# Kernel tuning notes

Measured on AMD Instinct MI355X. Metric: run time of the kernel, lower is better.

The kernel has to match this reference:

```python
import jax, jax.numpy as jnp
import numpy as np

NEG_BIG = -9e15
ALPHA = 0.2  # LeakyReLU negative slope
B, N, F_IN, F_OUT = 8, 2048, 128, 128


def setup_inputs() -> dict:
    key = jax.random.key(0)
    k1, k2, k3, k4 = jax.random.split(key, 4)
    inp = jax.random.normal(k1, (B, N, F_IN), dtype=jnp.float32)
    adj = jax.random.randint(k2, (B, N, N), 0, 2, dtype=jnp.int32)
    W = 0.02 * jax.random.normal(k3, (F_OUT, F_IN), dtype=jnp.float32)  # nn.Linear weight [out,in]
    a = 0.02 * jax.random.normal(k4, (1, 2 * F_OUT), dtype=jnp.float32)  # attention vector [1, 2F]
    return {"input": inp, "adj": adj, "W": W, "a": a}


def reference(input, adj, W, a):
    # h = input @ W^T : [B, N, F_OUT]
    h = jnp.einsum("bnf,of->bno", input, W)
    f_out = h.shape[-1]
    # Decompose a . [h_i || h_j] = (h_i . a1) + (h_j . a2) -- same math as the
    # explicit repeat_interleave/repeat/cat, without the O(N^2 * 2F) tensor.
    a1 = a[0, :f_out]
    a2 = a[0, f_out:]
    s1 = h @ a1  # [B, N] score for source node i
    s2 = h @ a2  # [B, N] score for target node j
    e = jax.nn.leaky_relu(s1[:, :, None] + s2[:, None, :], negative_slope=ALPHA)  # [B,N,N]
    masked = jnp.where(adj > 0, e, NEG_BIG)
    attention = jax.nn.softmax(masked, axis=-1)
    # dropout p=0.0 (eval) -> identity
    h_prime = jnp.einsum("bnm,bmo->bno", attention, h)
    return h_prime
```

## Files before the change

kernel.cpp:

```cpp
#include <hip/hip_runtime.h>
#include <stdint.h>


#define B_ 8
#define N_ 2048
#define FD 128
#define ALPHA_ 0.2f
#define TJ 128
#define NCHUNK (N_ / TJ)

typedef __attribute__((ext_vector_type(8))) short short8;
typedef __attribute__((ext_vector_type(4))) float f32x4;

#define HCHUNK(o, jc) ((((o) * 16) + ((jc) ^ ((o) & 15))) * 8)

__device__ __forceinline__ float bf2f(unsigned short u) {
    union { uint32_t i; float f; } v; v.i = ((uint32_t)u) << 16; return v.f;
}
__device__ __forceinline__ unsigned short f2bf(float f) {
    union { float f; uint32_t i; } v; v.f = f;
    uint32_t x = v.i;
    uint32_t r = (x + 0x7fffu + ((x >> 16) & 1u)) >> 16;
    return (unsigned short)r;
}

__global__ __launch_bounds__(256) void gat_h(
    const float* __restrict__ x,
    const float* __restrict__ W,
    const float* __restrict__ a,
    unsigned short* __restrict__ hT,
    float* __restrict__ s1o, float* __restrict__ s2o)
{
    __shared__ __align__(16) unsigned short Wlds[FD * FD];

    const int bid = blockIdx.x;
    const int tid = threadIdx.x;
    const int w = tid >> 6;
    const int lane = tid & 63;
    const int m = lane & 15;
    const int quad = lane >> 4;
    const int arow = bid * 64 + w * 16 + m;

#pragma unroll
    for (int it = 0; it < 8; it++) {
        int cid = it * 256 + tid;
        int o = cid >> 4, kc = cid & 15;
        const float* wp = W + (size_t)o * FD + kc * 8;
        float4 w0 = *(const float4*)wp;
        float4 w1 = *(const float4*)(wp + 4);
        uint4 pk;
        pk.x = (uint32_t)f2bf(w0.x) | ((uint32_t)f2bf(w0.y) << 16);
        pk.y = (uint32_t)f2bf(w0.z) | ((uint32_t)f2bf(w0.w) << 16);
        pk.z = (uint32_t)f2bf(w1.x) | ((uint32_t)f2bf(w1.y) << 16);
        pk.w = (uint32_t)f2bf(w1.z) | ((uint32_t)f2bf(w1.w) << 16);
        *(uint4*)&Wlds[HCHUNK(o, kc)] = pk;
    }
    __syncthreads();

    f32x4 acc[8];
#pragma unroll
    for (int ot = 0; ot < 8; ot++) acc[ot] = (f32x4){0.f, 0.f, 0.f, 0.f};

#pragma unroll
    for (int ks = 0; ks < 4; ks++) {
        const float* xp = x + (size_t)arow * FD + ks * 32 + quad * 8;
        float4 x0 = *(const float4*)xp;
        float4 x1 = *(const float4*)(xp + 4);
        float xv[8] = {x0.x, x0.y, x0.z, x0.w, x1.x, x1.y, x1.z, x1.w};
        union { unsigned short us[8]; short8 v; } ahi, alo;
#pragma unroll
        for (int jj = 0; jj < 8; jj++) {
            unsigned short hi = f2bf(xv[jj]);
            ahi.us[jj] = hi;
            alo.us[jj] = f2bf(xv[jj] - bf2f(hi));
        }
#pragma unroll
        for (int ot = 0; ot < 8; ot++) {
            union { uint4 u; short8 v; } bw;
            bw.u = *(const uint4*)&Wlds[HCHUNK(ot * 16 + m, ks * 4 + quad)];
            acc[ot] = __builtin_amdgcn_mfma_f32_16x16x32_bf16(ahi.v, bw.v, acc[ot], 0, 0, 0);
            acc[ot] = __builtin_amdgcn_mfma_f32_16x16x32_bf16(alo.v, bw.v, acc[ot], 0, 0, 0);
        }
    }

    const int rc0 = bid * 64 + w * 16 + quad * 4;
    const int bb = rc0 >> 11;
    const int jb = rc0 & (N_ - 1);
    unsigned short* hTb = hT + (size_t)bb * FD * N_;
    float s1p[4] = {0.f, 0.f, 0.f, 0.f};
    float s2p[4] = {0.f, 0.f, 0.f, 0.f};
#pragma unroll
    for (int ot = 0; ot < 8; ot++) {
        const int o = ot * 16 + m;
        uint32_t p0 = (uint32_t)f2bf(acc[ot][0]) | ((uint32_t)f2bf(acc[ot][1]) << 16);
        uint32_t p1 = (uint32_t)f2bf(acc[ot][2]) | ((uint32_t)f2bf(acc[ot][3]) << 16);
        *(uint32_t*)(hTb + (size_t)o * N_ + jb)     = p0;
        *(uint32_t*)(hTb + (size_t)o * N_ + jb + 2) = p1;
        float a1v = a[o], a2v = a[FD + o];
#pragma unroll
        for (int r = 0; r < 4; r++) {
            s1p[r] += acc[ot][r] * a1v;
            s2p[r] += acc[ot][r] * a2v;
        }
    }
#pragma unroll
    for (int off = 8; off >= 1; off >>= 1) {
#pragma unroll
        for (int r = 0; r < 4; r++) {
            s1p[r] += __shfl_xor(s1p[r], off);
            s2p[r] += __shfl_xor(s2p[r], off);
        }
    }
    if (m == 0) {
#pragma unroll
        for (int r = 0; r < 4; r++) {
            s1o[rc0 + r] = s1p[r];
            s2o[rc0 + r] = s2p[r];
        }
    }
}

__global__ __launch_bounds__(256) void gat_attn(
    const int* __restrict__ adj,
    const unsigned short* __restrict__ hT,
    const float* __restrict__ s1,
    const float* __restrict__ s2,
    float* __restrict__ out)
{
    __shared__ __align__(16) unsigned short hbuf[2][FD * TJ];
    __shared__ __align__(16) float s2s[N_];

    const int bid = blockIdx.x;
    const int b = bid >> 6;
    const int i0 = (bid & 63) * 32;
    const int tid = threadIdx.x;
    const int lane = tid & 63;
    const int w = tid >> 6;
    const int m = lane & 15;
    const int quad = lane >> 4;
    const int ihalf = w >> 1;
    const int ohalf = w & 1;

    const int irow = i0 + ihalf * 16 + m;
    const float s1v = s1[b * N_ + irow];
    const int* adjrow = adj + ((size_t)(b * N_ + irow)) * N_;
    const unsigned short* hTb = hT + (size_t)b * FD * N_;
    const float* s2b = s2 + b * N_;

#pragma unroll
    for (int it = 0; it < 2; it++) {
        int i4 = it * 256 + tid;
        *(float4*)&s2s[i4 * 4] = *(const float4*)(s2b + i4 * 4);
    }
    int4 acur[8];
#pragma unroll
    for (int ks = 0; ks < 4; ks++) {
        acur[2 * ks]     = *(const int4*)(adjrow + ks * 32 + quad * 8);
        acur[2 * ks + 1] = *(const int4*)(adjrow + ks * 32 + quad * 8 + 4);
    }
    {
        uint4 g[8];
#pragma unroll
        for (int it = 0; it < 8; it++) {
            int cid = it * 256 + tid;
            int o = cid >> 4, jc = cid & 15;
            g[it] = *(const uint4*)(hTb + (size_t)o * N_ + jc * 8);
        }
#pragma unroll
        for (int it = 0; it < 8; it++) {
            int cid = it * 256 + tid;
            int o = cid >> 4, jc = cid & 15;
            *(uint4*)&hbuf[0][HCHUNK(o, jc)] = g[it];
        }
    }
    __syncthreads();

    f32x4 acc[4];
#pragma unroll
    for (int t4 = 0; t4 < 4; t4++) acc[t4] = (f32x4){0.f, 0.f, 0.f, 0.f};
    float rs_loc = 0.f;

    for (int k = 0; k < NCHUNK; k++) {
        const int buf = k & 1;
        const bool more = (k + 1 < NCHUNK);
        int4 anext[8];
        uint4 gn[8];
        if (more) {
            const int j1 = (k + 1) * TJ;
#pragma unroll
            for (int ks = 0; ks < 4; ks++) {
                anext[2 * ks]     = *(const int4*)(adjrow + j1 + ks * 32 + quad * 8);
                anext[2 * ks + 1] = *(const int4*)(adjrow + j1 + ks * 32 + quad * 8 + 4);
            }
#pragma unroll
            for (int it = 0; it < 8; it++) {
                int cid = it * 256 + tid;
                int o = cid >> 4, jc = cid & 15;
                gn[it] = *(const uint4*)(hTb + (size_t)o * N_ + j1 + jc * 8);
            }
        }

#pragma unroll
        for (int ks = 0; ks < 4; ks++) {
            float4 sa = *(const float4*)&s2s[k * TJ + ks * 32 + quad * 8];
            float4 sb = *(const float4*)&s2s[k * TJ + ks * 32 + quad * 8 + 4];
            float sarr[8] = {sa.x, sa.y, sa.z, sa.w, sb.x, sb.y, sb.z, sb.w};
            int4 A0 = acur[2 * ks], A1 = acur[2 * ks + 1];
            int aarr[8] = {A0.x, A0.y, A0.z, A0.w, A1.x, A1.y, A1.z, A1.w};
            union { unsigned short us[8]; short8 v; } af;
#pragma unroll
            for (int jj = 0; jj < 8; jj++) {
                float e = s1v + sarr[jj];
                e = (e > 0.f) ? e : (ALPHA_ * e);
                float p = (aarr[jj] > 0) ? __expf(e) : 0.f;
                rs_loc += p;
                af.us[jj] = f2bf(p);
            }
#pragma unroll
            for (int t4 = 0; t4 < 4; t4++) {
                const int o = (ohalf * 4 + t4) * 16 + m;
                union { uint4 u; short8 v; } bf;
                bf.u = *(const uint4*)&hbuf[buf][HCHUNK(o, ks * 4 + quad)];
                acc[t4] = __builtin_amdgcn_mfma_f32_16x16x32_bf16(af.v, bf.v, acc[t4], 0, 0, 0);
            }
        }

        if (more) {
#pragma unroll
            for (int it = 0; it < 8; it++) {
                int cid = it * 256 + tid;
                int o = cid >> 4, jc = cid & 15;
                *(uint4*)&hbuf[buf ^ 1][HCHUNK(o, jc)] = gn[it];
            }
            __syncthreads();
#pragma unroll
            for (int q = 0; q < 8; q++) acur[q] = anext[q];
        }
    }

    rs_loc += __shfl_xor(rs_loc, 16);
    rs_loc += __shfl_xor(rs_loc, 32);
    float rinv[4];
#pragma unroll
    for (int r = 0; r < 4; r++) rinv[r] = 1.0f / __shfl(rs_loc, quad * 4 + r);

    float* outp = out + (size_t)(b * N_ + i0 + ihalf * 16) * FD;
#pragma unroll
    for (int t4 = 0; t4 < 4; t4++) {
        const int col = (ohalf * 4 + t4) * 16 + m;
#pragma unroll
        for (int r = 0; r < 4; r++) {
            outp[(size_t)(quad * 4 + r) * FD + col] = acc[t4][r] * rinv[r];
        }
    }
}

extern "C" void kernel_launch(void* const* d_in, const int* in_sizes, int n_in,
                              void* d_out, int out_size, void* d_ws, size_t ws_size,
                              hipStream_t stream) {
    const void* xv = d_in[0];
    const void* adjv = d_in[1];
    const void* Wv = d_in[2];
    const void* av = d_in[3];
    for (int i = 0; i < n_in; i++) {
        switch (in_sizes[i]) {
            case 2097152:  xv = d_in[i]; break;
            case 33554432: adjv = d_in[i]; break;
            case 16384:    Wv = d_in[i]; break;
            case 256:      av = d_in[i]; break;
            default: break;
        }
    }
    const float* x = (const float*)xv;
    const int* adj = (const int*)adjv;
    const float* W = (const float*)Wv;
    const float* a = (const float*)av;
    float* out = (float*)d_out;

    char* p = (char*)d_ws;
    unsigned short* hT = (unsigned short*)p;  p += (size_t)B_ * FD * N_ * 2;
    float* s1 = (float*)p;                    p += (size_t)B_ * N_ * 4;
    float* s2 = (float*)p;

    gat_h<<<256, 256, 0, stream>>>(x, W, a, hT, s1, s2);
    gat_attn<<<512, 256, 0, stream>>>(adj, hT, s1, s2, out);
}
```

Measured before the change: 225.3 us.

## Pre-swizzle hT into chunked LDS layout and shrink attention blocks to two waves

The h projection kernel now writes hT in a chunked, pre-swizzled layout of 64-column blocks, so the attention kernel can copy each chunk into LDS with plain contiguous uint4 loads instead of strided per-row gathers. The attention kernel drops to 128 threads, each wave covering all 128 output columns for its 16 rows, with a 64-column j tile. It reads s2 straight from global memory instead of staging it in LDS. This reduces LDS use and address arithmetic and removes redundant score/exp computation across the output halves. The trade-offs are more accumulator registers per wave, fewer waves per block, and twice as many loop iterations and barriers.

```diff
diff --git a/kernel.cpp b/kernel.cpp
--- a/kernel.cpp
+++ b/kernel.cpp
@@ -6,13 +6,15 @@
 #define N_ 2048
 #define FD 128
 #define ALPHA_ 0.2f
-#define TJ 128
+#define TJ 64
 #define NCHUNK (N_ / TJ)
+#define CHUNK_U4 1024
 
 typedef __attribute__((ext_vector_type(8))) short short8;
 typedef __attribute__((ext_vector_type(4))) float f32x4;
 
 #define HCHUNK(o, jc) ((((o) * 16) + ((jc) ^ ((o) & 15))) * 8)
+#define HC64(o, jc) ((o) * 8 + ((jc) ^ ((o) & 7)))
 
 __device__ __forceinline__ float bf2f(unsigned short u) {
     union { uint32_t i; float f; } v; v.i = ((uint32_t)u) << 16; return v.f;
@@ -86,16 +88,19 @@
     const int rc0 = bid * 64 + w * 16 + quad * 4;
     const int bb = rc0 >> 11;
     const int jb = rc0 & (N_ - 1);
-    unsigned short* hTb = hT + (size_t)bb * FD * N_;
+    const int kc = jb >> 6;
+    const int jcl = (jb & 63) >> 3;
+    const int off = jb & 7;
+    unsigned short* hTb = hT + (size_t)bb * FD * N_ + (size_t)kc * (CHUNK_U4 * 8);
     float s1p[4] = {0.f, 0.f, 0.f, 0.f};
     float s2p[4] = {0.f, 0.f, 0.f, 0.f};
 #pragma unroll
     for (int ot = 0; ot < 8; ot++) {
         const int o = ot * 16 + m;
-        uint32_t p0 = (uint32_t)f2bf(acc[ot][0]) | ((uint32_t)f2bf(acc[ot][1]) << 16);
-        uint32_t p1 = (uint32_t)f2bf(acc[ot][2]) | ((uint32_t)f2bf(acc[ot][3]) << 16);
-        *(uint32_t*)(hTb + (size_t)o * N_ + jb)     = p0;
-        *(uint32_t*)(hTb + (size_t)o * N_ + jb + 2) = p1;
+        uint2 pk;
+        pk.x = (uint32_t)f2bf(acc[ot][0]) | ((uint32_t)f2bf(acc[ot][1]) << 16);
+        pk.y = (uint32_t)f2bf(acc[ot][2]) | ((uint32_t)f2bf(acc[ot][3]) << 16);
+        *(uint2*)(hTb + (size_t)HC64(o, jcl) * 8 + off) = pk;
         float a1v = a[o], a2v = a[FD + o];
 #pragma unroll
         for (int r = 0; r < 4; r++) {
@@ -104,11 +109,11 @@
         }
     }
 #pragma unroll
-    for (int off = 8; off >= 1; off >>= 1) {
-#pragma unroll
-        for (int r = 0; r < 4; r++) {
-            s1p[r] += __shfl_xor(s1p[r], off);
-            s2p[r] += __shfl_xor(s2p[r], off);
+    for (int offx = 8; offx >= 1; offx >>= 1) {
+#pragma unroll
+        for (int r = 0; r < 4; r++) {
+            s1p[r] += __shfl_xor(s1p[r], offx);
+            s2p[r] += __shfl_xor(s2p[r], offx);
         }
     }
     if (m == 0) {
@@ -120,15 +125,14 @@
     }
 }
 
-__global__ __launch_bounds__(256) void gat_attn(
+__global__ __launch_bounds__(128) void gat_attn(
     const int* __restrict__ adj,
     const unsigned short* __restrict__ hT,
     const float* __restrict__ s1,
     const float* __restrict__ s2,
     float* __restrict__ out)
 {
-    __shared__ __align__(16) unsigned short hbuf[2][FD * TJ];
-    __shared__ __align__(16) float s2s[N_];
+    __shared__ __align__(16) uint4 hbuf[2][CHUNK_U4];
 
     const int bid = blockIdx.x;
     const int b = bid >> 6;
@@ -138,72 +142,54 @@
     const int w = tid >> 6;
     const int m = lane & 15;
     const int quad = lane >> 4;
-    const int ihalf = w >> 1;
-    const int ohalf = w & 1;
-
-    const int irow = i0 + ihalf * 16 + m;
+
+    const int irow = i0 + w * 16 + m;
     const float s1v = s1[b * N_ + irow];
     const int* adjrow = adj + ((size_t)(b * N_ + irow)) * N_;
-    const unsigned short* hTb = hT + (size_t)b * FD * N_;
+    const uint4* hTc = (const uint4*)(hT + (size_t)b * FD * N_);
     const float* s2b = s2 + b * N_;
 
-#pragma unroll
-    for (int it = 0; it < 2; it++) {
-        int i4 = it * 256 + tid;
-        *(float4*)&s2s[i4 * 4] = *(const float4*)(s2b + i4 * 4);
-    }
-    int4 acur[8];
-#pragma unroll
-    for (int ks = 0; ks < 4; ks++) {
+    int4 acur[4];
+#pragma unroll
+    for (int ks = 0; ks < 2; ks++) {
         acur[2 * ks]     = *(const int4*)(adjrow + ks * 32 + quad * 8);
         acur[2 * ks + 1] = *(const int4*)(adjrow + ks * 32 + quad * 8 + 4);
     }
     {
         uint4 g[8];
 #pragma unroll
-        for (int it = 0; it < 8; it++) {
-            int cid = it * 256 + tid;
-            int o = cid >> 4, jc = cid & 15;
-            g[it] = *(const uint4*)(hTb + (size_t)o * N_ + jc * 8);
-        }
-#pragma unroll
-        for (int it = 0; it < 8; it++) {
-            int cid = it * 256 + tid;
-            int o = cid >> 4, jc = cid & 15;
-            *(uint4*)&hbuf[0][HCHUNK(o, jc)] = g[it];
-        }
+        for (int it = 0; it < 8; it++) g[it] = hTc[it * 128 + tid];
+#pragma unroll
+        for (int it = 0; it < 8; it++) hbuf[0][it * 128 + tid] = g[it];
     }
     __syncthreads();
 
-    f32x4 acc[4];
-#pragma unroll
-    for (int t4 = 0; t4 < 4; t4++) acc[t4] = (f32x4){0.f, 0.f, 0.f, 0.f};
+    f32x4 acc[8];
+#pragma unroll
+    for (int ot = 0; ot < 8; ot++) acc[ot] = (f32x4){0.f, 0.f, 0.f, 0.f};
     float rs_loc = 0.f;
 
     for (int k = 0; k < NCHUNK; k++) {
         const int buf = k & 1;
         const bool more = (k + 1 < NCHUNK);
-        int4 anext[8];
+        int4 anext[4];
         uint4 gn[8];
         if (more) {
             const int j1 = (k + 1) * TJ;
 #pragma unroll
-            for (int ks = 0; ks < 4; ks++) {
+            for (int ks = 0; ks < 2; ks++) {
                 anext[2 * ks]     = *(const int4*)(adjrow + j1 + ks * 32 + quad * 8);
                 anext[2 * ks + 1] = *(const int4*)(adjrow + j1 + ks * 32 + quad * 8 + 4);
             }
 #pragma unroll
-            for (int it = 0; it < 8; it++) {
-                int cid = it * 256 + tid;
-                int o = cid >> 4, jc = cid & 15;
-                gn[it] = *(const uint4*)(hTb + (size_t)o * N_ + j1 + jc * 8);
-            }
-        }
-
-#pragma unroll
-        for (int ks = 0; ks < 4; ks++) {
-            float4 sa = *(const float4*)&s2s[k * TJ + ks * 32 + quad * 8];
-            float4 sb = *(const float4*)&s2s[k * TJ + ks * 32 + quad * 8 + 4];
+            for (int it = 0; it < 8; it++)
+                gn[it] = hTc[(size_t)(k + 1) * CHUNK_U4 + it * 128 + tid];
+        }
+
+#pragma unroll
+        for (int ks = 0; ks < 2; ks++) {
+            float4 sa = *(const float4*)(s2b + k * TJ + ks * 32 + quad * 8);
+            float4 sb = *(const float4*)(s2b + k * TJ + ks * 32 + quad * 8 + 4);
             float sarr[8] = {sa.x, sa.y, sa.z, sa.w, sb.x, sb.y, sb.z, sb.w};
             int4 A0 = acur[2 * ks], A1 = acur[2 * ks + 1];
             int aarr[8] = {A0.x, A0.y, A0.z, A0.w, A1.x, A1.y, A1.z, A1.w};
@@ -216,25 +202,22 @@
                 rs_loc += p;
                 af.us[jj] = f2bf(p);
             }
-#pragma unroll
-            for (int t4 = 0; t4 < 4; t4++) {
-                const int o = (ohalf * 4 + t4) * 16 + m;
+            const int jc = ks * 4 + quad;
+#pragma unroll
+            for (int ot = 0; ot < 8; ot++) {
+                const int o = ot * 16 + m;
                 union { uint4 u; short8 v; } bf;
-                bf.u = *(const uint4*)&hbuf[buf][HCHUNK(o, ks * 4 + quad)];
-                acc[t4] = __builtin_amdgcn_mfma_f32_16x16x32_bf16(af.v, bf.v, acc[t4], 0, 0, 0);
+                bf.u = *(const uint4*)&hbuf[buf][HC64(o, jc)];
+                acc[ot] = __builtin_amdgcn_mfma_f32_16x16x32_bf16(af.v, bf.v, acc[ot], 0, 0, 0);
             }
         }
 
         if (more) {
 #pragma unroll
-            for (int it = 0; it < 8; it++) {
-                int cid = it * 256 + tid;
-                int o = cid >> 4, jc = cid & 15;
-                *(uint4*)&hbuf[buf ^ 1][HCHUNK(o, jc)] = gn[it];
-            }
+            for (int it = 0; it < 8; it++) hbuf[buf ^ 1][it * 128 + tid] = gn[it];
             __syncthreads();
 #pragma unroll
-            for (int q = 0; q < 8; q++) acur[q] = anext[q];
+            for (int q = 0; q < 4; q++) acur[q] = anext[q];
         }
     }
 
@@ -244,13 +227,13 @@
 #pragma unroll
     for (int r = 0; r < 4; r++) rinv[r] = 1.0f / __shfl(rs_loc, quad * 4 + r);
 
-    float* outp = out + (size_t)(b * N_ + i0 + ihalf * 16) * FD;
-#pragma unroll
-    for (int t4 = 0; t4 < 4; t4++) {
-        const int col = (ohalf * 4 + t4) * 16 + m;
-#pragma unroll
-        for (int r = 0; r < 4; r++) {
-            outp[(size_t)(quad * 4 + r) * FD + col] = acc[t4][r] * rinv[r];
+    float* outp = out + (size_t)(b * N_ + i0 + w * 16) * FD;
+#pragma unroll
+    for (int ot = 0; ot < 8; ot++) {
+        const int col = ot * 16 + m;
+#pragma unroll
+        for (int r = 0; r < 4; r++) {
+            outp[(size_t)(quad * 4 + r) * FD + col] = acc[ot][r] * rinv[r];
         }
     }
 }
@@ -283,5 +266,5 @@
     float* s2 = (float*)p;
 
     gat_h<<<256, 256, 0, stream>>>(x, W, a, hT, s1, s2);
-    gat_attn<<<512, 256, 0, stream>>>(adj, hT, s1, s2, out);
-}
+    gat_attn<<<512, 128, 0, stream>>>(adj, hT, s1, s2, out);
+}
```

After: 252.1 us. +11.9%, slower.
